# Optimization experiments

Measured on AMD Instinct MI355X. Metric: run time of the kernel, lower is better.

## Reference

```python
import jax, jax.numpy as jnp
import numpy as np

MAG = 1.0
TAU = 0.5
B, D, C = 8192, 256, 128


def setup_inputs() -> dict:
    key = jax.random.key(0)
    k1, k2 = jax.random.split(key)
    outputs = jax.random.normal(k1, (B, D), dtype=jnp.float32)
    labels = jax.random.normal(k2, (B, C), dtype=jnp.float32)
    return {"outputs": outputs, "labels": labels}


def reference(outputs, labels):
    # Cosine-similarity matrix of labels, min-max normalized to [0, 1]
    norm2labels = labels / (jnp.linalg.norm(labels, axis=1, keepdims=True) + 1e-12)
    sim_mat = norm2labels @ norm2labels.T  # [B, B]
    sim_mat = (sim_mat - sim_mat.min()) / (sim_mat.max() - sim_mat.min())

    # Pairwise Euclidean distances of outputs via the Gram trick
    # ||x_i - x_j||^2 = ||x_i||^2 + ||x_j||^2 - 2 <x_i, x_j>
    sq = jnp.sum(outputs * outputs, axis=1)  # [B]
    d2 = sq[:, None] + sq[None, :] - 2.0 * (outputs @ outputs.T)  # [B, B]
    d2 = jnp.maximum(d2, 0.0)
    nz = d2 > 0.0
    # safe sqrt: zero (diagonal) entries get distance 0 with zero gradient,
    # matching torch.norm's subgradient at 0
    eud = jnp.sqrt(jnp.where(nz, d2, 1.0)) * nz
    eud = eud / eud.max()

    distance = eud + sim_mat  # [B, B]
    pos_mask = sim_mat > TAU

    # Per-row masked log-sum-exp terms (distance in [0, 2], no overflow risk)
    pos_loss = jnp.log(jnp.sum(jnp.where(pos_mask, jnp.exp(distance), 0.0), axis=1))
    neg_loss = jnp.log(jnp.sum(jnp.where(pos_mask, 0.0, jnp.exp(MAG - distance)), axis=1))

    # clamp negatives (and -inf from empty masks) to 0, as the original `if < 0` does
    loss = jnp.maximum(pos_loss, 0.0) + jnp.maximum(neg_loss, 0.0)
    return jnp.mean(loss)
```

## Files before the change

kernel.cpp:

```cpp
#include <hip/hip_runtime.h>
#include <hip/hip_bf16.h>


#define B_N 8192
#define NT   64
#define TILE 128
#define NTRI 2080
#define WS_NEEDED 142704704ull

typedef __attribute__((ext_vector_type(8))) short bf16x8;
typedef __attribute__((ext_vector_type(4))) float f32x4;
typedef __attribute__((ext_vector_type(2))) _Float16 f16x2;
typedef __attribute__((ext_vector_type(4))) unsigned u32x4;

typedef const __attribute__((address_space(1))) void g_void;
typedef __attribute__((address_space(3))) void l_void;

__device__ __forceinline__ unsigned fenc(float f) {
    unsigned u = __float_as_uint(f);
    return (u & 0x80000000u) ? ~u : (u | 0x80000000u);
}
__device__ __forceinline__ float fdec(unsigned k) {
    unsigned u = (k & 0x80000000u) ? (k ^ 0x80000000u) : ~k;
    return __uint_as_float(u);
}
__device__ __forceinline__ unsigned pack2(float a, float b) {
    f16x2 p; p[0] = (_Float16)a; p[1] = (_Float16)b;
    return *(unsigned*)&p;
}

__device__ __forceinline__ void tile_decode(int b, int& bi, int& bj) {
    int si, sj, ti, tj;
    if (b < 544) {
        int sb = b / 136, w = b - sb * 136;
        int i = 0;
        while (w >= 16 - i) { w -= 16 - i; i++; }
        si = sb; sj = sb; ti = i; tj = i + w;
    } else {
        int q = (b - 544) >> 8, w = (b - 544) & 255;
        int i = 0;
        while (q >= 3 - i) { q -= 3 - i; i++; }
        si = i; sj = i + 1 + q;
        ti = w >> 4; tj = w & 15;
    }
    bi = si * 16 + ti; bj = sj * 16 + tj;
}

__global__ __launch_bounds__(256) void prep_kernel(
    const float* __restrict__ outputs, const float* __restrict__ labels,
    __hip_bfloat16* __restrict__ Obp, __hip_bfloat16* __restrict__ Lnp,
    float* __restrict__ sq, float* __restrict__ pos_sums,
    float* __restrict__ neg_sums, unsigned* __restrict__ stats) {
    int g = blockIdx.x, tid = threadIdx.x;
    int rl = tid >> 4, c = tid & 15;
    int row = g * 16 + rl;
    __shared__ __align__(16) short tO[16][264];
    __shared__ __align__(16) short tL[16][136];

    float s = 0.f;
    #pragma unroll
    for (int k = 0; k < 4; k++) {
        f32x4 v = *(const f32x4*)&outputs[(size_t)row * 256 + c * 16 + k * 4];
        s += v[0]*v[0] + v[1]*v[1] + v[2]*v[2] + v[3]*v[3];
        __hip_bfloat16 b4[4];
        #pragma unroll
        for (int i = 0; i < 4; i++) b4[i] = __float2bfloat16(v[i]);
        *(uint2*)&tO[rl][c * 16 + k * 4] = *(uint2*)b4;
    }
    #pragma unroll
    for (int m = 1; m < 16; m <<= 1) s += __shfl_xor(s, m);
    if (c == 0) sq[row] = s;

    float ls = 0.f;
    f32x4 u0 = *(const f32x4*)&labels[(size_t)row * 128 + c * 8];
    f32x4 u1 = *(const f32x4*)&labels[(size_t)row * 128 + c * 8 + 4];
    ls += u0[0]*u0[0] + u0[1]*u0[1] + u0[2]*u0[2] + u0[3]*u0[3];
    ls += u1[0]*u1[0] + u1[1]*u1[1] + u1[2]*u1[2] + u1[3]*u1[3];
    #pragma unroll
    for (int m = 1; m < 16; m <<= 1) ls += __shfl_xor(ls, m);
    float inv = 1.f / (sqrtf(ls) + 1e-12f);
    {
        __hip_bfloat16 b4[4];
        #pragma unroll
        for (int i = 0; i < 4; i++) b4[i] = __float2bfloat16(u0[i] * inv);
        *(uint2*)&tL[rl][c * 8] = *(uint2*)b4;
        #pragma unroll
        for (int i = 0; i < 4; i++) b4[i] = __float2bfloat16(u1[i] * inv);
        *(uint2*)&tL[rl][c * 8 + 4] = *(uint2*)b4;
    }
    if (tid < 16) { pos_sums[g * 16 + tid] = 0.f; neg_sums[g * 16 + tid] = 0.f; }
    if (g == 0 && tid == 0) {
        stats[0] = 0xFFFFFFFFu; stats[1] = 0u; stats[2] = 0u;
    }
    __syncthreads();

    #pragma unroll
    for (int q = 0; q < 2; q++) {
        int sl = tid * 2 + q;
        int o = sl >> 4, rr = sl & 15;
        uint4 d = *(uint4*)&tO[rr][o * 8];
        *(uint4*)&Obp[(size_t)g * 4096 + (size_t)sl * 8] = d;
    }
    {
        int o = tid >> 4, rr = tid & 15;
        uint4 d = *(uint4*)&tL[rr][o * 8];
        *(uint4*)&Lnp[(size_t)g * 2048 + (size_t)tid * 8] = d;
    }
}

template<int KD8>
__device__ __forceinline__ void stage_slice(
    const short* __restrict__ P, int g0, int o0, short* L, int tid) {
    #pragma unroll
    for (int p = 0; p < 4; p++) {
        int u = p * 256 + tid;
        int gl = u >> 7, off = u & 127;
        size_t gu = ((size_t)(g0 + gl) * KD8 + o0) * 16 + off;
        __builtin_amdgcn_global_load_lds((g_void*)(P + gu * 8),
                                         (l_void*)(L + (size_t)u * 8), 16, 0, 0);
    }
}

__device__ __forceinline__ void mfma_slice(
    const short* As, const short* Bs, int wm4, int wn4,
    int l15, int quad, f32x4 (&acc)[4][4]) {
    #pragma unroll
    for (int kc = 0; kc < 2; kc++) {
        bf16x8 a[4], b[4];
        #pragma unroll
        for (int mi = 0; mi < 4; mi++)
            a[mi] = *(const bf16x8*)&As[((wm4 + mi) * 128
                                         + (kc * 4 + quad) * 16 + l15) * 8];
        #pragma unroll
        for (int ni = 0; ni < 4; ni++)
            b[ni] = *(const bf16x8*)&Bs[((wn4 + ni) * 128
                                         + (kc * 4 + quad) * 16 + l15) * 8];
        #pragma unroll
        for (int mi = 0; mi < 4; mi++)
            #pragma unroll
            for (int ni = 0; ni < 4; ni++)
                acc[mi][ni] = __builtin_amdgcn_mfma_f32_16x16x32_bf16(
                    a[mi], b[ni], acc[mi][ni], 0, 0, 0);
    }
}

__device__ __forceinline__ void zero_acc(f32x4 (&acc)[4][4]) {
    #pragma unroll
    for (int mi = 0; mi < 4; mi++)
        #pragma unroll
        for (int ni = 0; ni < 4; ni++) {
            f32x4 z = {0.f, 0.f, 0.f, 0.f};
            acc[mi][ni] = z;
        }
}

template<int KD8, int NS>
__device__ __forceinline__ void gram_staged(
    const short* __restrict__ P, int gA0, int gB0,
    short* As, short* Bs, int tid, int wm4, int wn4,
    int l15, int quad, f32x4 (&acc)[4][4]) {
    #pragma unroll
    for (int s = 0; s < NS; s++) {
        __syncthreads();
        stage_slice<KD8>(P, gA0, s * 8, As, tid);
        stage_slice<KD8>(P, gB0, s * 8, Bs, tid);
        __syncthreads();
        mfma_slice(As, Bs, wm4, wn4, l15, quad, acc);
    }
}

__global__ __launch_bounds__(256, 2) void stats_kernel(
    const short* __restrict__ Lnp, const short* __restrict__ Obp,
    const float* __restrict__ sq, unsigned* __restrict__ stats,
    unsigned* __restrict__ simT, unsigned* __restrict__ eudT, int store) {
    int bi, bj;
    tile_decode(blockIdx.x, bi, bj);
    int tid = threadIdx.x, lane = tid & 63, wid = tid >> 6;
    int wm = (wid >> 1) * 64, wn = (wid & 1) * 64;
    int wm4 = (wid >> 1) * 4, wn4 = (wid & 1) * 4;
    int l15 = lane & 15, quad = lane >> 4;
    int rB = bi * TILE, cB = bj * TILE;
    size_t tB = (size_t)blockIdx.x * 8192 + (size_t)tid * 4;

    __shared__ __align__(16) short As[1024 * 8];
    __shared__ __align__(16) short Bs[1024 * 8];

    float lmin = 1e30f, lmax = -1e30f, dmax = 0.f;
    f32x4 acc[4][4];

    zero_acc(acc);
    gram_staged<16, 2>(Lnp, bi * 8, bj * 8, As, Bs, tid, wm4, wn4, l15, quad, acc);
    #pragma unroll
    for (int mi = 0; mi < 4; mi++) {
        u32x4 v0, v1;
        #pragma unroll
        for (int ni = 0; ni < 4; ni++)
            #pragma unroll
            for (int h = 0; h < 2; h++) {
                float s0 = acc[mi][ni][2 * h], s1 = acc[mi][ni][2 * h + 1];
                lmin = fminf(lmin, fminf(s0, s1));
                lmax = fmaxf(lmax, fmaxf(s0, s1));
                int j = ni * 2 + h;
                unsigned pk = pack2(s0, s1);
                if (j < 4) v0[j] = pk; else v1[j - 4] = pk;
            }
        if (store) {
            __builtin_nontemporal_store(v0, (u32x4*)(simT + tB + (mi * 2 + 0) * 1024));
            __builtin_nontemporal_store(v1, (u32x4*)(simT + tB + (mi * 2 + 1) * 1024));
        }
    }

    zero_acc(acc);
    gram_staged<32, 4>(Obp, bi * 8, bj * 8, As, Bs, tid, wm4, wn4, l15, quad, acc);
    float sqj[4];
    #pragma unroll
    for (int ni = 0; ni < 4; ni++) sqj[ni] = sq[cB + wn + ni * 16 + l15];
    #pragma unroll
    for (int mi = 0; mi < 4; mi++) {
        f32x4 sqi = *(const f32x4*)&sq[rB + wm + mi * 16 + quad * 4];
        u32x4 v0, v1;
        #pragma unroll
        for (int ni = 0; ni < 4; ni++)
            #pragma unroll
            for (int h = 0; h < 2; h++) {
                float d20 = fmaxf(sqi[2*h]   + sqj[ni] - 2.f * acc[mi][ni][2*h],   0.f);
                float d21 = fmaxf(sqi[2*h+1] + sqj[ni] - 2.f * acc[mi][ni][2*h+1], 0.f);
                dmax = fmaxf(dmax, fmaxf(d20, d21));
                float e0 = (d20 > 0.f) ? sqrtf(d20) : 0.f;
                float e1 = (d21 > 0.f) ? sqrtf(d21) : 0.f;
                int j = ni * 2 + h;
                unsigned pk = pack2(e0, e1);
                if (j < 4) v0[j] = pk; else v1[j - 4] = pk;
            }
        if (store) {
            __builtin_nontemporal_store(v0, (u32x4*)(eudT + tB + (mi * 2 + 0) * 1024));
            __builtin_nontemporal_store(v1, (u32x4*)(eudT + tB + (mi * 2 + 1) * 1024));
        }
    }

    #pragma unroll
    for (int m = 1; m < 64; m <<= 1) {
        lmin = fminf(lmin, __shfl_xor(lmin, m));
        lmax = fmaxf(lmax, __shfl_xor(lmax, m));
        dmax = fmaxf(dmax, __shfl_xor(dmax, m));
    }
    __shared__ float red[3][4];
    if ((tid & 63) == 0) { red[0][wid] = lmin; red[1][wid] = lmax; red[2][wid] = dmax; }
    __syncthreads();
    if (tid == 0) {
        lmin = fminf(fminf(red[0][0], red[0][1]), fminf(red[0][2], red[0][3]));
        lmax = fmaxf(fmaxf(red[1][0], red[1][1]), fmaxf(red[1][2], red[1][3]));
        dmax = fmaxf(fmaxf(red[2][0], red[2][1]), fmaxf(red[2][2], red[2][3]));
        atomicMin(&stats[0], fenc(lmin));
        atomicMax(&stats[1], fenc(lmax));
        atomicMax(&stats[2], fenc(dmax));
    }
}

__global__ __launch_bounds__(256) void loss_stream_kernel(
    const unsigned* __restrict__ simT, const unsigned* __restrict__ eudT,
    const unsigned* __restrict__ stats,
    float* __restrict__ pos_sums, float* __restrict__ neg_sums) {
    int bi, bj;
    tile_decode(blockIdx.x, bi, bj);
    int tid = threadIdx.x, lane = tid & 63, wid = tid >> 6;
    int wm = (wid >> 1) * 64, wn = (wid & 1) * 64;
    int l15 = lane & 15, quad = lane >> 4;
    size_t tB = (size_t)blockIdx.x * 8192 + (size_t)tid * 4;

    float smin = fdec(stats[0]);
    float smax = fdec(stats[1]);
    float d2max = fdec(stats[2]);
    float invr = 1.f / (smax - smin);
    float invem = rsqrtf(d2max);

    __shared__ float rP[TILE][2], rN[TILE][2];
    __shared__ float cP[TILE][2], cN[TILE][2];
    float cpsum[4] = {0.f, 0.f, 0.f, 0.f};
    float cnsum[4] = {0.f, 0.f, 0.f, 0.f};

    #pragma unroll
    for (int mi = 0; mi < 4; mi++) {
        u32x4 s0 = __builtin_nontemporal_load((const u32x4*)(simT + tB + (mi * 2 + 0) * 1024));
        u32x4 s1 = __builtin_nontemporal_load((const u32x4*)(simT + tB + (mi * 2 + 1) * 1024));
        u32x4 e0 = __builtin_nontemporal_load((const u32x4*)(eudT + tB + (mi * 2 + 0) * 1024));
        u32x4 e1 = __builtin_nontemporal_load((const u32x4*)(eudT + tB + (mi * 2 + 1) * 1024));
        float ps[4] = {0.f, 0.f, 0.f, 0.f};
        float ns[4] = {0.f, 0.f, 0.f, 0.f};
        #pragma unroll
        for (int j = 0; j < 8; j++) {
            unsigned sv = (j < 4) ? s0[j] : s1[j - 4];
            unsigned ev = (j < 4) ? e0[j] : e1[j - 4];
            int ni = j >> 1, h = j & 1;
            f16x2 spair = *(f16x2*)&sv;
            f16x2 epair = *(f16x2*)&ev;
            #pragma unroll
            for (int e = 0; e < 2; e++) {
                float sn = ((float)spair[e] - smin) * invr;
                float dist = (float)epair[e] * invem + sn;
                bool pos = sn > 0.5f;
                float pv = pos ? __expf(dist) : 0.f;
                float nv = pos ? 0.f : __expf(1.0f - dist);
                ps[2 * h + e] += pv;  ns[2 * h + e] += nv;
                cpsum[ni] += pv;  cnsum[ni] += nv;
            }
        }
        #pragma unroll
        for (int r = 0; r < 4; r++) {
            #pragma unroll
            for (int m = 1; m < 16; m <<= 1) {
                ps[r] += __shfl_xor(ps[r], m);
                ns[r] += __shfl_xor(ns[r], m);
            }
            if (l15 == 0) {
                int rr = wm + mi * 16 + quad * 4 + r;
                rP[rr][wid & 1] = ps[r];
                rN[rr][wid & 1] = ns[r];
            }
        }
    }
    #pragma unroll
    for (int ni = 0; ni < 4; ni++) {
        #pragma unroll
        for (int m = 16; m < 64; m <<= 1) {
            cpsum[ni] += __shfl_xor(cpsum[ni], m);
            cnsum[ni] += __shfl_xor(cnsum[ni], m);
        }
        if (quad == 0) {
            int cc = wn + ni * 16 + l15;
            cP[cc][wid >> 1] = cpsum[ni];
            cN[cc][wid >> 1] = cnsum[ni];
        }
    }
    __syncthreads();
    if (tid < TILE) {
        atomicAdd(&pos_sums[bi * TILE + tid], rP[tid][0] + rP[tid][1]);
        atomicAdd(&neg_sums[bi * TILE + tid], rN[tid][0] + rN[tid][1]);
        if (bi != bj) {
            atomicAdd(&pos_sums[bj * TILE + tid], cP[tid][0] + cP[tid][1]);
            atomicAdd(&neg_sums[bj * TILE + tid], cN[tid][0] + cN[tid][1]);
        }
    }
}

__global__ __launch_bounds__(256, 2) void loss_recompute_kernel(
    const short* __restrict__ Lnp, const short* __restrict__ Obp,
    const float* __restrict__ sq, const unsigned* __restrict__ stats,
    float* __restrict__ pos_sums, float* __restrict__ neg_sums) {
    int bi, bj;
    tile_decode(blockIdx.x, bi, bj);
    int tid = threadIdx.x, lane = tid & 63, wid = tid >> 6;
    int wm = (wid >> 1) * 64, wn = (wid & 1) * 64;
    int wm4 = (wid >> 1) * 4, wn4 = (wid & 1) * 4;
    int l15 = lane & 15, quad = lane >> 4;
    int rB = bi * TILE, cB = bj * TILE;

    __shared__ __align__(16) short As[1024 * 8];
    __shared__ __align__(16) short Bs[1024 * 8];
    __shared__ unsigned simW[256 * 33];
    __shared__ float rP[TILE][2], rN[TILE][2];
    __shared__ float cP[TILE][2], cN[TILE][2];
    unsigned* my = &simW[tid * 33];

    f32x4 acc[4][4];

    zero_acc(acc);
    gram_staged<16, 2>(Lnp, bi * 8, bj * 8, As, Bs, tid, wm4, wn4, l15, quad, acc);
    #pragma unroll
    for (int mi = 0; mi < 4; mi++)
        #pragma unroll
        for (int ni = 0; ni < 4; ni++) {
            my[(mi * 4 + ni) * 2 + 0] = pack2(acc[mi][ni][0], acc[mi][ni][1]);
            my[(mi * 4 + ni) * 2 + 1] = pack2(acc[mi][ni][2], acc[mi][ni][3]);
        }

    zero_acc(acc);
    gram_staged<32, 4>(Obp, bi * 8, bj * 8, As, Bs, tid, wm4, wn4, l15, quad, acc);

    float smin = fdec(stats[0]);
    float smax = fdec(stats[1]);
    float d2max = fdec(stats[2]);
    float invr = 1.f / (smax - smin);
    float invem = rsqrtf(d2max);

    float sqj[4];
    #pragma unroll
    for (int ni = 0; ni < 4; ni++) sqj[ni] = sq[cB + wn + ni * 16 + l15];
    float cpsum[4] = {0.f, 0.f, 0.f, 0.f};
    float cnsum[4] = {0.f, 0.f, 0.f, 0.f};

    #pragma unroll
    for (int mi = 0; mi < 4; mi++) {
        f32x4 sqi = *(const f32x4*)&sq[rB + wm + mi * 16 + quad * 4];
        float ps[4] = {0.f, 0.f, 0.f, 0.f};
        float ns[4] = {0.f, 0.f, 0.f, 0.f};
        #pragma unroll
        for (int ni = 0; ni < 4; ni++) {
            f16x2 s01 = ((const f16x2*)my)[(mi * 4 + ni) * 2 + 0];
            f16x2 s23 = ((const f16x2*)my)[(mi * 4 + ni) * 2 + 1];
            #pragma unroll
            for (int r = 0; r < 4; r++) {
                float sraw = (r < 2) ? (float)s01[r] : (float)s23[r - 2];
                float sn = (sraw - smin) * invr;
                float g = acc[mi][ni][r];
                float d2 = fmaxf(sqi[r] + sqj[ni] - 2.f * g, 0.f);
                float eud = (d2 > 0.f) ? sqrtf(d2) * invem : 0.f;
                float dist = eud + sn;
                bool pos = sn > 0.5f;
                float pv = pos ? __expf(dist) : 0.f;
                float nv = pos ? 0.f : __expf(1.0f - dist);
                ps[r] += pv;  ns[r] += nv;
                cpsum[ni] += pv;  cnsum[ni] += nv;
            }
        }
        #pragma unroll
        for (int r = 0; r < 4; r++) {
            #pragma unroll
            for (int m = 1; m < 16; m <<= 1) {
                ps[r] += __shfl_xor(ps[r], m);
                ns[r] += __shfl_xor(ns[r], m);
            }
            if (l15 == 0) {
                int rr = wm + mi * 16 + quad * 4 + r;
                rP[rr][wid & 1] = ps[r];
                rN[rr][wid & 1] = ns[r];
            }
        }
    }
    #pragma unroll
    for (int ni = 0; ni < 4; ni++) {
        #pragma unroll
        for (int m = 16; m < 64; m <<= 1) {
            cpsum[ni] += __shfl_xor(cpsum[ni], m);
            cnsum[ni] += __shfl_xor(cnsum[ni], m);
        }
        if (quad == 0) {
            int cc = wn + ni * 16 + l15;
            cP[cc][wid >> 1] = cpsum[ni];
            cN[cc][wid >> 1] = cnsum[ni];
        }
    }
    __syncthreads();
    if (tid < TILE) {
        atomicAdd(&pos_sums[bi * TILE + tid], rP[tid][0] + rP[tid][1]);
        atomicAdd(&neg_sums[bi * TILE + tid], rN[tid][0] + rN[tid][1]);
        if (bi != bj) {
            atomicAdd(&pos_sums[bj * TILE + tid], cP[tid][0] + cP[tid][1]);
            atomicAdd(&neg_sums[bj * TILE + tid], cN[tid][0] + cN[tid][1]);
        }
    }
}

__global__ __launch_bounds__(256) void finalize_kernel(
    const float* __restrict__ pos_sums, const float* __restrict__ neg_sums,
    float* __restrict__ out) {
    int t = threadIdx.x;
    float acc = 0.f;
    for (int i = t; i < B_N; i += 256) {
        float p = pos_sums[i], n = neg_sums[i];
        float pl = fmaxf(logf(p), 0.f);
        float nl = (n > 0.f) ? fmaxf(logf(n), 0.f) : 0.f;
        acc += pl + nl;
    }
    #pragma unroll
    for (int m = 1; m < 64; m <<= 1) acc += __shfl_xor(acc, m);
    __shared__ float w4[4];
    if ((t & 63) == 0) w4[t >> 6] = acc;
    __syncthreads();
    if (t == 0) out[0] = (w4[0] + w4[1] + w4[2] + w4[3]) / (float)B_N;
}

extern "C" void kernel_launch(void* const* d_in, const int* in_sizes, int n_in,
                              void* d_out, int out_size, void* d_ws, size_t ws_size,
                              hipStream_t stream) {
    const float* outputs = (const float*)d_in[0];
    const float* labels  = (const float*)d_in[1];
    float* out = (float*)d_out;
    char* ws = (char*)d_ws;
    __hip_bfloat16* Obp = (__hip_bfloat16*)(ws);
    __hip_bfloat16* Lnp = (__hip_bfloat16*)(ws + 4194304);
    float* sq           = (float*)(ws + 6291456);
    float* pos_sums     = (float*)(ws + 6324224);
    float* neg_sums     = (float*)(ws + 6356992);
    unsigned* stats     = (unsigned*)(ws + 6389760);
    unsigned* simT      = (unsigned*)(ws + 6389824);
    unsigned* eudT      = (unsigned*)(ws + 74547264);
    int big = (ws_size >= WS_NEEDED) ? 1 : 0;

    prep_kernel<<<B_N / 16, 256, 0, stream>>>(outputs, labels, Obp, Lnp, sq,
                                              pos_sums, neg_sums, stats);
    stats_kernel<<<NTRI, 256, 0, stream>>>((const short*)Lnp, (const short*)Obp,
                                           sq, stats, simT, eudT, big);
    if (big)
        loss_stream_kernel<<<NTRI, 256, 0, stream>>>(simT, eudT, stats,
                                                     pos_sums, neg_sums);
    else
        loss_recompute_kernel<<<NTRI, 256, 0, stream>>>((const short*)Lnp,
                                                        (const short*)Obp,
                                                        sq, stats,
                                                        pos_sums, neg_sums);
    finalize_kernel<<<1, 256, 0, stream>>>(pos_sums, neg_sums, out);
}
```

Baseline: 209.6 us.

## Software-pipeline Gram staging with 4-slot LDS ring and direct global-to-LDS loads

Replaces the synchronous stage-then-compute loop in the stats kernel with a 4-deep ring of LDS buffers filled via global_load_lds, using explicit vmcnt waits and barriers. Loads for the outputs Gram are issued while the label Gram and its epilogue still run, so global latency can hide behind MFMA and store work. The store flag becomes a template parameter so the vmcnt counts can account for the nontemporal stores. LDS use grows to 64KB per block, which may limit the two-blocks-per-CU occupancy, and the hand-tuned wait counts are fragile.

```diff
diff --git a/kernel.cpp b/kernel.cpp
--- a/kernel.cpp
+++ b/kernel.cpp
@@ -3,7 +3,6 @@
 
 
 #define B_N 8192
-#define NT   64
 #define TILE 128
 #define NTRI 2080
 #define WS_NEEDED 142704704ull
@@ -169,10 +168,46 @@
     }
 }
 
+template<int KD8>
+__device__ __forceinline__ void stage32(const short* __restrict__ P, int g0,
+                                        int ko8, short* L, int tid) {
+    #pragma unroll
+    for (int p = 0; p < 2; p++) {
+        int u = p * 256 + tid;
+        int gl = u >> 6, k8l = (u >> 4) & 3, r = u & 15;
+        size_t gu = ((size_t)(g0 + gl) * KD8 + ko8 + k8l) * 16 + r;
+        __builtin_amdgcn_global_load_lds((g_void*)(P + gu * 8),
+                                         (l_void*)(L + (size_t)u * 8), 16, 0, 0);
+    }
+}
+
+__device__ __forceinline__ void mfma_slice32(
+    const short* As, const short* Bs, int wm4, int wn4,
+    int l15, int quad, f32x4 (&acc)[4][4]) {
+    bf16x8 a[4], b[4];
+    #pragma unroll
+    for (int mi = 0; mi < 4; mi++)
+        a[mi] = *(const bf16x8*)&As[((wm4 + mi) * 64 + quad * 16 + l15) * 8];
+    #pragma unroll
+    for (int ni = 0; ni < 4; ni++)
+        b[ni] = *(const bf16x8*)&Bs[((wn4 + ni) * 64 + quad * 16 + l15) * 8];
+    #pragma unroll
+    for (int mi = 0; mi < 4; mi++)
+        #pragma unroll
+        for (int ni = 0; ni < 4; ni++)
+            acc[mi][ni] = __builtin_amdgcn_mfma_f32_16x16x32_bf16(
+                a[mi], b[ni], acc[mi][ni], 0, 0, 0);
+}
+
+#define VMCNT(n) asm volatile("s_waitcnt vmcnt(" #n ")" ::: "memory")
+#define BAR() __builtin_amdgcn_s_barrier()
+#define FENCE() asm volatile("" ::: "memory")
+
+template<int STORE>
 __global__ __launch_bounds__(256, 2) void stats_kernel(
     const short* __restrict__ Lnp, const short* __restrict__ Obp,
     const float* __restrict__ sq, unsigned* __restrict__ stats,
-    unsigned* __restrict__ simT, unsigned* __restrict__ eudT, int store) {
+    unsigned* __restrict__ simT, unsigned* __restrict__ eudT) {
     int bi, bj;
     tile_decode(blockIdx.x, bi, bj);
     int tid = threadIdx.x, lane = tid & 63, wid = tid >> 6;
@@ -180,16 +215,38 @@
     int wm4 = (wid >> 1) * 4, wn4 = (wid & 1) * 4;
     int l15 = lane & 15, quad = lane >> 4;
     int rB = bi * TILE, cB = bj * TILE;
+    int g8 = bi * 8, h8 = bj * 8;
     size_t tB = (size_t)blockIdx.x * 8192 + (size_t)tid * 4;
 
-    __shared__ __align__(16) short As[1024 * 8];
-    __shared__ __align__(16) short Bs[1024 * 8];
+    __shared__ __align__(16) short As[4][4096];
+    __shared__ __align__(16) short Bs[4][4096];
+    __shared__ float red[3][4];
 
     float lmin = 1e30f, lmax = -1e30f, dmax = 0.f;
     f32x4 acc[4][4];
 
     zero_acc(acc);
-    gram_staged<16, 2>(Lnp, bi * 8, bj * 8, As, Bs, tid, wm4, wn4, l15, quad, acc);
+    stage32<16>(Lnp, g8, 0,  &As[0][0], tid); stage32<16>(Lnp, h8, 0,  &Bs[0][0], tid);
+    stage32<16>(Lnp, g8, 4,  &As[1][0], tid); stage32<16>(Lnp, h8, 4,  &Bs[1][0], tid);
+    stage32<16>(Lnp, g8, 8,  &As[2][0], tid); stage32<16>(Lnp, h8, 8,  &Bs[2][0], tid);
+    stage32<16>(Lnp, g8, 12, &As[3][0], tid); stage32<16>(Lnp, h8, 12, &Bs[3][0], tid);
+
+    VMCNT(12); BAR();
+    mfma_slice32(&As[0][0], &Bs[0][0], wm4, wn4, l15, quad, acc);
+    BAR();
+    stage32<32>(Obp, g8, 0, &As[0][0], tid); stage32<32>(Obp, h8, 0, &Bs[0][0], tid);
+    VMCNT(12); BAR();
+    mfma_slice32(&As[1][0], &Bs[1][0], wm4, wn4, l15, quad, acc);
+    BAR();
+    stage32<32>(Obp, g8, 4, &As[1][0], tid); stage32<32>(Obp, h8, 4, &Bs[1][0], tid);
+    VMCNT(12); BAR();
+    mfma_slice32(&As[2][0], &Bs[2][0], wm4, wn4, l15, quad, acc);
+    BAR();
+    stage32<32>(Obp, g8, 8, &As[2][0], tid); stage32<32>(Obp, h8, 8, &Bs[2][0], tid);
+
+    VMCNT(12); BAR();
+    mfma_slice32(&As[3][0], &Bs[3][0], wm4, wn4, l15, quad, acc);
+    FENCE();
     #pragma unroll
     for (int mi = 0; mi < 4; mi++) {
         u32x4 v0, v1;
@@ -204,20 +261,58 @@
                 unsigned pk = pack2(s0, s1);
                 if (j < 4) v0[j] = pk; else v1[j - 4] = pk;
             }
-        if (store) {
+        if (STORE) {
             __builtin_nontemporal_store(v0, (u32x4*)(simT + tB + (mi * 2 + 0) * 1024));
             __builtin_nontemporal_store(v1, (u32x4*)(simT + tB + (mi * 2 + 1) * 1024));
         }
     }
-
+    FENCE();
+    BAR();
+    stage32<32>(Obp, g8, 12, &As[3][0], tid); stage32<32>(Obp, h8, 12, &Bs[3][0], tid);
     zero_acc(acc);
-    gram_staged<32, 4>(Obp, bi * 8, bj * 8, As, Bs, tid, wm4, wn4, l15, quad, acc);
-    float sqj[4];
+
+    if (STORE) { VMCNT(20); } else { VMCNT(12); }
+    BAR();
+    mfma_slice32(&As[0][0], &Bs[0][0], wm4, wn4, l15, quad, acc);
+    BAR();
+    stage32<32>(Obp, g8, 16, &As[0][0], tid); stage32<32>(Obp, h8, 16, &Bs[0][0], tid);
+    if (STORE) { VMCNT(20); } else { VMCNT(12); }
+    BAR();
+    mfma_slice32(&As[1][0], &Bs[1][0], wm4, wn4, l15, quad, acc);
+    BAR();
+    stage32<32>(Obp, g8, 20, &As[1][0], tid); stage32<32>(Obp, h8, 20, &Bs[1][0], tid);
+    if (STORE) { VMCNT(20); } else { VMCNT(12); }
+    BAR();
+    mfma_slice32(&As[2][0], &Bs[2][0], wm4, wn4, l15, quad, acc);
+    BAR();
+    stage32<32>(Obp, g8, 24, &As[2][0], tid); stage32<32>(Obp, h8, 24, &Bs[2][0], tid);
+
+    VMCNT(12); BAR();
+    mfma_slice32(&As[3][0], &Bs[3][0], wm4, wn4, l15, quad, acc);
+    BAR();
+    stage32<32>(Obp, g8, 28, &As[3][0], tid); stage32<32>(Obp, h8, 28, &Bs[3][0], tid);
+
+    VMCNT(12); BAR();
+    mfma_slice32(&As[0][0], &Bs[0][0], wm4, wn4, l15, quad, acc);
+    BAR();
+    float sqj[4]; f32x4 sqi4[4];
     #pragma unroll
     for (int ni = 0; ni < 4; ni++) sqj[ni] = sq[cB + wn + ni * 16 + l15];
     #pragma unroll
+    for (int mi = 0; mi < 4; mi++)
+        sqi4[mi] = *(const f32x4*)&sq[rB + wm + mi * 16 + quad * 4];
+    VMCNT(16); BAR();
+    mfma_slice32(&As[1][0], &Bs[1][0], wm4, wn4, l15, quad, acc);
+    BAR();
+    VMCNT(12); BAR();
+    mfma_slice32(&As[2][0], &Bs[2][0], wm4, wn4, l15, quad, acc);
+    BAR();
+    VMCNT(8); BAR();
+    mfma_slice32(&As[3][0], &Bs[3][0], wm4, wn4, l15, quad, acc);
+
+    #pragma unroll
     for (int mi = 0; mi < 4; mi++) {
-        f32x4 sqi = *(const f32x4*)&sq[rB + wm + mi * 16 + quad * 4];
+        f32x4 sqi = sqi4[mi];
         u32x4 v0, v1;
         #pragma unroll
         for (int ni = 0; ni < 4; ni++)
@@ -232,7 +327,7 @@
                 unsigned pk = pack2(e0, e1);
                 if (j < 4) v0[j] = pk; else v1[j - 4] = pk;
             }
-        if (store) {
+        if (STORE) {
             __builtin_nontemporal_store(v0, (u32x4*)(eudT + tB + (mi * 2 + 0) * 1024));
             __builtin_nontemporal_store(v1, (u32x4*)(eudT + tB + (mi * 2 + 1) * 1024));
         }
@@ -244,7 +339,6 @@
         lmax = fmaxf(lmax, __shfl_xor(lmax, m));
         dmax = fmaxf(dmax, __shfl_xor(dmax, m));
     }
-    __shared__ float red[3][4];
     if ((tid & 63) == 0) { red[0][wid] = lmin; red[1][wid] = lmax; red[2][wid] = dmax; }
     __syncthreads();
     if (tid == 0) {
@@ -489,15 +583,20 @@
 
     prep_kernel<<<B_N / 16, 256, 0, stream>>>(outputs, labels, Obp, Lnp, sq,
                                               pos_sums, neg_sums, stats);
-    stats_kernel<<<NTRI, 256, 0, stream>>>((const short*)Lnp, (const short*)Obp,
-                                           sq, stats, simT, eudT, big);
-    if (big)
+    if (big) {
+        stats_kernel<1><<<NTRI, 256, 0, stream>>>((const short*)Lnp,
+                                                  (const short*)Obp,
+                                                  sq, stats, simT, eudT);
         loss_stream_kernel<<<NTRI, 256, 0, stream>>>(simT, eudT, stats,
                                                      pos_sums, neg_sums);
-    else
+    } else {
+        stats_kernel<0><<<NTRI, 256, 0, stream>>>((const short*)Lnp,
+                                                  (const short*)Obp,
+                                                  sq, stats, simT, eudT);
         loss_recompute_kernel<<<NTRI, 256, 0, stream>>>((const short*)Lnp,
                                                         (const short*)Obp,
                                                         sq, stats,
                                                         pos_sums, neg_sums);
+    }
     finalize_kernel<<<1, 256, 0, stream>>>(pos_sums, neg_sums, out);
 }
```

Result: no change. 209.1 us (-0.2%).
